# Optimization experiments

Measured on AMD Instinct MI355X. Metric: run time of the kernel, lower is better.

The kernel has to match this reference:

```python
import jax, jax.numpy as jnp
import numpy as np

N = 200000
E = 600000
H = 128
NUM_EDGE_TYPES = 16
LN_EPS = 1e-5


def setup_inputs() -> dict:
    key = jax.random.key(0)
    ks = jax.random.split(key, 10)
    x = jax.random.normal(ks[0], (N, H), dtype=jnp.float32)
    edge_index = jax.random.randint(ks[1], (2, E), 0, N, dtype=jnp.int32)
    edge_types = jax.random.randint(ks[2], (E,), 0, NUM_EDGE_TYPES, dtype=jnp.int32)
    s = 1.0 / np.sqrt(H)
    edge_emb = jax.random.normal(ks[3], (NUM_EDGE_TYPES, H), dtype=jnp.float32)
    W_self = jax.random.uniform(ks[4], (H, H), dtype=jnp.float32, minval=-s, maxval=s)
    b_self = jax.random.uniform(ks[5], (H,), dtype=jnp.float32, minval=-s, maxval=s)
    W_msg = jax.random.uniform(ks[6], (H, H), dtype=jnp.float32, minval=-s, maxval=s)
    b_msg = jax.random.uniform(ks[7], (H,), dtype=jnp.float32, minval=-s, maxval=s)
    gamma = jnp.ones((H,), dtype=jnp.float32)
    beta = jnp.zeros((H,), dtype=jnp.float32)
    return {
        "x": x, "edge_index": edge_index, "edge_types": edge_types,
        "edge_emb": edge_emb, "W_self": W_self, "b_self": b_self,
        "W_msg": W_msg, "b_msg": b_msg, "gamma": gamma, "beta": beta,
    }


def reference(x, edge_index, edge_types, edge_emb, W_self, b_self, W_msg, b_msg, gamma, beta):
    src = edge_index[0]
    dst = edge_index[1]
    # gather source node features + typed edge embedding: [E, H]
    typed_messages = x[src] + edge_emb[edge_types]
    # scatter-add into destination nodes: [N, H]
    aggregated = jnp.zeros_like(x).at[dst].add(typed_messages)
    # linear epilogue (torch Linear: y = x @ W.T + b)
    out = (x @ W_self.T + b_self) + (aggregated @ W_msg.T + b_msg)
    out = jax.nn.relu(out)
    # LayerNorm over last dim
    mu = jnp.mean(out, axis=-1, keepdims=True)
    var = jnp.mean(jnp.square(out - mu), axis=-1, keepdims=True)
    out = (out - mu) * jax.lax.rsqrt(var + LN_EPS) * gamma + beta
    # dropout is identity in eval mode
    return out
```

## Files before the change

kernel.cpp:

```cpp
#include <hip/hip_runtime.h>
#include <stdint.h>

#define H 128
#define TM 16
#define MAXDEG 24

typedef __attribute__((ext_vector_type(8))) short short8;
typedef __attribute__((ext_vector_type(4))) float f32x4;
typedef __attribute__((ext_vector_type(4))) int i32x4;

__device__ __forceinline__ unsigned short f2bf(float f) {
    union { float f; unsigned u; } v; v.f = f;
    unsigned u = v.u;
    u += 0x7fffu + ((u >> 16) & 1u);
    return (unsigned short)(u >> 16);
}

__device__ __forceinline__ float bf2f(unsigned short u) {
    union { unsigned u; float f; } v; v.u = ((unsigned)u) << 16; return v.f;
}

__device__ __forceinline__ short8 cvt8(f32x4 a, f32x4 b) {
    short8 r;
    r[0] = (short)f2bf(a.x); r[1] = (short)f2bf(a.y);
    r[2] = (short)f2bf(a.z); r[3] = (short)f2bf(a.w);
    r[4] = (short)f2bf(b.x); r[5] = (short)f2bf(b.y);
    r[6] = (short)f2bf(b.z); r[7] = (short)f2bf(b.w);
    return r;
}

__global__ __launch_bounds__(256) void prep_kernel(
    const float* __restrict__ x, const float* __restrict__ emb,
    unsigned short* __restrict__ xb, unsigned short* __restrict__ embb,
    const int* __restrict__ ei, const int* __restrict__ et,
    int* __restrict__ cnt, int* __restrict__ bucket,
    int total8x, int total8e, int E)
{
    int i = blockIdx.x * 256 + threadIdx.x;
    if (i < total8x) {
        f32x4 a = ((const f32x4*)x)[2 * i];
        f32x4 b = ((const f32x4*)x)[2 * i + 1];
        ((short8*)xb)[i] = cvt8(a, b);
    } else if (i < total8x + total8e) {
        int j = i - total8x;
        f32x4 a = ((const f32x4*)emb)[2 * j];
        f32x4 b = ((const f32x4*)emb)[2 * j + 1];
        ((short8*)embb)[j] = cvt8(a, b);
    }
    if (i < E) {
        int src = ei[i];
        int dst = ei[E + i];
        int t   = et[i];
        int pos = atomicAdd(&cnt[dst], 1);
        if (pos < MAXDEG) bucket[(size_t)dst * MAXDEG + pos] = src | (t << 18);
    }
}

template<bool EMB_LDS>
__global__ __launch_bounds__(256) void fused_gemm_kernel(
    const unsigned short* __restrict__ xb, const unsigned short* __restrict__ embb,
    const int* __restrict__ cnt, const int* __restrict__ bucket,
    const int* __restrict__ ei, const int* __restrict__ et,
    const float* __restrict__ Wself, const float* __restrict__ bself,
    const float* __restrict__ Wmsg, const float* __restrict__ bmsg,
    const float* __restrict__ gamma, const float* __restrict__ beta,
    float* __restrict__ out, int nTiles, int E, int T)
{
    __shared__ __align__(16) short a_stage[TM * 264];
    __shared__ __align__(16) float o_stage[TM * 132];
    __shared__ __align__(16) short emb_s[16 * 136];

    const int tid  = threadIdx.x;
    const int wave = tid >> 6;
    const int lane = tid & 63;
    const int col  = lane & 15;
    const int quad = lane >> 4;
    const int node = tid >> 4;
    const int l    = tid & 15;

    if (EMB_LDS && tid < T * 16) {
        int t = tid >> 4;
        *(short8*)&emb_s[t * 136 + l * 8] = *(const short8*)(embb + t * H + l * 8);
    }

    short8 bfrag[2][8];
    float bias[2];
#pragma unroll
    for (int s = 0; s < 2; ++s) {
        const int h = (wave * 2 + s) * 16 + col;
        bias[s] = bself[h] + bmsg[h];
#pragma unroll
        for (int kst = 0; kst < 8; ++kst) {
            const float* W = (kst < 4) ? Wself : Wmsg;
            const int k0 = (kst & 3) * 32 + quad * 8;
            const float* p = W + (size_t)h * H + k0;
            f32x4 w0 = *(const f32x4*)(p);
            f32x4 w1 = *(const f32x4*)(p + 4);
            bfrag[s][kst] = cvt8(w0, w1);
        }
    }

    const int f0 = l * 8;
    f32x4 g0  = *(const f32x4*)(gamma + f0);
    f32x4 g1  = *(const f32x4*)(gamma + f0 + 4);
    f32x4 be0 = *(const f32x4*)(beta + f0);
    f32x4 be1 = *(const f32x4*)(beta + f0 + 4);

    __syncthreads();

    for (int tile = blockIdx.x; tile < nTiles; tile += gridDim.x) {
        const size_t row = (size_t)tile * TM + node;

        short8 xv_st = *(const short8*)(xb + row * H + l * 8);

        int c = cnt[row];
        float acc[8] = {0.f, 0.f, 0.f, 0.f, 0.f, 0.f, 0.f, 0.f};
        if (c <= MAXDEG) {
            const int* b = bucket + row * MAXDEG;
            for (int i0 = 0; i0 < c; i0 += 4) {
                i32x4 p = *(const i32x4*)(b + i0);
                int rem = c - i0;
                bool h1 = rem > 1, h2 = rem > 2, h3 = rem > 3;
                short8 xv0, xv1, xv2, xv3, ev0, ev1, ev2, ev3;
                {
                    int s = p.x & 0x3FFFF, t = p.x >> 18;
                    xv0 = *(const short8*)(xb + (size_t)s * H + l * 8);
                    ev0 = EMB_LDS ? *(const short8*)&emb_s[t * 136 + l * 8]
                                  : *(const short8*)(embb + (size_t)t * H + l * 8);
                }
                if (h1) {
                    int s = p.y & 0x3FFFF, t = p.y >> 18;
                    xv1 = *(const short8*)(xb + (size_t)s * H + l * 8);
                    ev1 = EMB_LDS ? *(const short8*)&emb_s[t * 136 + l * 8]
                                  : *(const short8*)(embb + (size_t)t * H + l * 8);
                }
                if (h2) {
                    int s = p.z & 0x3FFFF, t = p.z >> 18;
                    xv2 = *(const short8*)(xb + (size_t)s * H + l * 8);
                    ev2 = EMB_LDS ? *(const short8*)&emb_s[t * 136 + l * 8]
                                  : *(const short8*)(embb + (size_t)t * H + l * 8);
                }
                if (h3) {
                    int s = p.w & 0x3FFFF, t = p.w >> 18;
                    xv3 = *(const short8*)(xb + (size_t)s * H + l * 8);
                    ev3 = EMB_LDS ? *(const short8*)&emb_s[t * 136 + l * 8]
                                  : *(const short8*)(embb + (size_t)t * H + l * 8);
                }
#pragma unroll
                for (int j = 0; j < 8; ++j) acc[j] += bf2f((unsigned short)xv0[j]) + bf2f((unsigned short)ev0[j]);
                if (h1) {
#pragma unroll
                    for (int j = 0; j < 8; ++j) acc[j] += bf2f((unsigned short)xv1[j]) + bf2f((unsigned short)ev1[j]);
                }
                if (h2) {
#pragma unroll
                    for (int j = 0; j < 8; ++j) acc[j] += bf2f((unsigned short)xv2[j]) + bf2f((unsigned short)ev2[j]);
                }
                if (h3) {
#pragma unroll
                    for (int j = 0; j < 8; ++j) acc[j] += bf2f((unsigned short)xv3[j]) + bf2f((unsigned short)ev3[j]);
                }
            }
        } else {
            for (int e = 0; e < E; ++e) {
                if (ei[E + e] == (int)row) {
                    int s = ei[e], t = et[e];
                    short8 xv = *(const short8*)(xb + (size_t)s * H + l * 8);
                    short8 ev = EMB_LDS ? *(const short8*)&emb_s[t * 136 + l * 8]
                                        : *(const short8*)(embb + (size_t)t * H + l * 8);
#pragma unroll
                    for (int j = 0; j < 8; ++j) acc[j] += bf2f((unsigned short)xv[j]) + bf2f((unsigned short)ev[j]);
                }
            }
        }

        *(short8*)&a_stage[node * 264 + l * 8] = xv_st;
        short8 ar;
#pragma unroll
        for (int j = 0; j < 8; ++j) ar[j] = (short)f2bf(acc[j]);
        *(short8*)&a_stage[node * 264 + 128 + l * 8] = ar;
        __syncthreads();

        short8 afr[8];
#pragma unroll
        for (int kst = 0; kst < 8; ++kst)
            afr[kst] = *(const short8*)(&a_stage[col * 264 + kst * 32 + quad * 8]);

        f32x4 acc0 = {0.f, 0.f, 0.f, 0.f};
        f32x4 acc1 = {0.f, 0.f, 0.f, 0.f};
#pragma unroll
        for (int kst = 0; kst < 8; ++kst) {
            acc0 = __builtin_amdgcn_mfma_f32_16x16x32_bf16(afr[kst], bfrag[0][kst], acc0, 0, 0, 0);
            acc1 = __builtin_amdgcn_mfma_f32_16x16x32_bf16(afr[kst], bfrag[1][kst], acc1, 0, 0, 0);
        }

#pragma unroll
        for (int s = 0; s < 2; ++s) {
            const int h = (wave * 2 + s) * 16 + col;
            f32x4 a = s ? acc1 : acc0;
#pragma unroll
            for (int r = 0; r < 4; ++r) {
                const int m = quad * 4 + r;
                float v = a[r] + bias[s];
                o_stage[m * 132 + h] = v > 0.f ? v : 0.f;
            }
        }
        __syncthreads();

        float v[8];
        float s1 = 0.f, s2 = 0.f;
#pragma unroll
        for (int j = 0; j < 8; ++j) {
            v[j] = o_stage[node * 132 + f0 + j];
            s1 += v[j];
            s2 += v[j] * v[j];
        }
#pragma unroll
        for (int m = 1; m < 16; m <<= 1) {
            s1 += __shfl_xor(s1, m, 64);
            s2 += __shfl_xor(s2, m, 64);
        }
        const float mu = s1 * (1.f / 128.f);
        const float var = s2 * (1.f / 128.f) - mu * mu;
        const float rstd = rsqrtf(var + 1e-5f);

        f32x4 o0, o1;
        o0.x = (v[0] - mu) * rstd * g0.x + be0.x;
        o0.y = (v[1] - mu) * rstd * g0.y + be0.y;
        o0.z = (v[2] - mu) * rstd * g0.z + be0.z;
        o0.w = (v[3] - mu) * rstd * g0.w + be0.w;
        o1.x = (v[4] - mu) * rstd * g1.x + be1.x;
        o1.y = (v[5] - mu) * rstd * g1.y + be1.y;
        o1.z = (v[6] - mu) * rstd * g1.z + be1.z;
        o1.w = (v[7] - mu) * rstd * g1.w + be1.w;

        float* dst = out + row * H + f0;
        __builtin_nontemporal_store(o0, (f32x4*)dst);
        __builtin_nontemporal_store(o1, (f32x4*)(dst + 4));
    }
}

__global__ __launch_bounds__(256) void scatter_kernel(
    const float* __restrict__ x, const int* __restrict__ ei,
    const int* __restrict__ et, const float* __restrict__ emb,
    float* __restrict__ agg, int E)
{
    int g = blockIdx.x * 256 + threadIdx.x;
    int e = g >> 5;
    int l = g & 31;
    if (e >= E) return;
    int src = ei[e];
    int dst = ei[E + e];
    int t   = et[e];
    f32x4 xv = *(const f32x4*)(x   + (size_t)src * H + l * 4);
    f32x4 ev = *(const f32x4*)(emb + (size_t)t   * H + l * 4);
    float* b = agg + (size_t)dst * H + l * 4;
    atomicAdd(b + 0, xv.x + ev.x);
    atomicAdd(b + 1, xv.y + ev.y);
    atomicAdd(b + 2, xv.z + ev.z);
    atomicAdd(b + 3, xv.w + ev.w);
}

__global__ __launch_bounds__(256) void gemm_ln_f32_kernel(
    const float* __restrict__ x,
    const float* __restrict__ Wself, const float* __restrict__ bself,
    const float* __restrict__ Wmsg, const float* __restrict__ bmsg,
    const float* __restrict__ gamma, const float* __restrict__ beta,
    float* __restrict__ out, int nTiles)
{
    __shared__ __align__(16) short a_stage[TM * 264];
    __shared__ __align__(16) float o_stage[TM * 132];

    const int tid  = threadIdx.x;
    const int wave = tid >> 6;
    const int lane = tid & 63;
    const int col  = lane & 15;
    const int quad = lane >> 4;

    short8 bfrag[2][8];
    float bias[2];
#pragma unroll
    for (int s = 0; s < 2; ++s) {
        const int h = (wave * 2 + s) * 16 + col;
        bias[s] = bself[h] + bmsg[h];
#pragma unroll
        for (int kst = 0; kst < 8; ++kst) {
            const float* W = (kst < 4) ? Wself : Wmsg;
            const int k0 = (kst & 3) * 32 + quad * 8;
            const float* p = W + (size_t)h * H + k0;
            f32x4 w0 = *(const f32x4*)(p);
            f32x4 w1 = *(const f32x4*)(p + 4);
            bfrag[s][kst] = cvt8(w0, w1);
        }
    }

    const int lnode = tid >> 4;
    const int f0 = (tid & 15) * 8;
    f32x4 g0  = *(const f32x4*)(gamma + f0);
    f32x4 g1  = *(const f32x4*)(gamma + f0 + 4);
    f32x4 be0 = *(const f32x4*)(beta + f0);
    f32x4 be1 = *(const f32x4*)(beta + f0 + 4);

    for (int tile = blockIdx.x; tile < nTiles; tile += gridDim.x) {
        const size_t rowBase = (size_t)tile * TM;
        {
            const int node = tid >> 4;
            const int seg  = tid & 15;
            const int k0   = seg * 16;
            const float* src = (seg < 8)
                ? (x   + (rowBase + node) * H + k0)
                : (out + (rowBase + node) * H + (k0 - 128));
            f32x4 v0 = ((const f32x4*)src)[0];
            f32x4 v1 = ((const f32x4*)src)[1];
            f32x4 v2 = ((const f32x4*)src)[2];
            f32x4 v3 = ((const f32x4*)src)[3];
            *(short8*)(&a_stage[node * 264 + k0])     = cvt8(v0, v1);
            *(short8*)(&a_stage[node * 264 + k0 + 8]) = cvt8(v2, v3);
        }
        __syncthreads();

        short8 afr[8];
#pragma unroll
        for (int kst = 0; kst < 8; ++kst)
            afr[kst] = *(const short8*)(&a_stage[col * 264 + kst * 32 + quad * 8]);

        f32x4 acc0 = {0.f, 0.f, 0.f, 0.f};
        f32x4 acc1 = {0.f, 0.f, 0.f, 0.f};
#pragma unroll
        for (int kst = 0; kst < 8; ++kst) {
            acc0 = __builtin_amdgcn_mfma_f32_16x16x32_bf16(afr[kst], bfrag[0][kst], acc0, 0, 0, 0);
            acc1 = __builtin_amdgcn_mfma_f32_16x16x32_bf16(afr[kst], bfrag[1][kst], acc1, 0, 0, 0);
        }

#pragma unroll
        for (int s = 0; s < 2; ++s) {
            const int h = (wave * 2 + s) * 16 + col;
            f32x4 a = s ? acc1 : acc0;
#pragma unroll
            for (int r = 0; r < 4; ++r) {
                const int m = quad * 4 + r;
                float v = a[r] + bias[s];
                o_stage[m * 132 + h] = v > 0.f ? v : 0.f;
            }
        }
        __syncthreads();

        float v[8];
        float s1 = 0.f, s2 = 0.f;
#pragma unroll
        for (int j = 0; j < 8; ++j) {
            v[j] = o_stage[lnode * 132 + f0 + j];
            s1 += v[j];
            s2 += v[j] * v[j];
        }
#pragma unroll
        for (int m = 1; m < 16; m <<= 1) {
            s1 += __shfl_xor(s1, m, 64);
            s2 += __shfl_xor(s2, m, 64);
        }
        const float mu = s1 * (1.f / 128.f);
        const float var = s2 * (1.f / 128.f) - mu * mu;
        const float rstd = rsqrtf(var + 1e-5f);

        f32x4 o0, o1;
        o0.x = (v[0] - mu) * rstd * g0.x + be0.x;
        o0.y = (v[1] - mu) * rstd * g0.y + be0.y;
        o0.z = (v[2] - mu) * rstd * g0.z + be0.z;
        o0.w = (v[3] - mu) * rstd * g0.w + be0.w;
        o1.x = (v[4] - mu) * rstd * g1.x + be1.x;
        o1.y = (v[5] - mu) * rstd * g1.y + be1.y;
        o1.z = (v[6] - mu) * rstd * g1.z + be1.z;
        o1.w = (v[7] - mu) * rstd * g1.w + be1.w;

        float* dst = out + (rowBase + lnode) * H + f0;
        *(f32x4*)(dst)     = o0;
        *(f32x4*)(dst + 4) = o1;
    }
}

extern "C" void kernel_launch(void* const* d_in, const int* in_sizes, int n_in,
                              void* d_out, int out_size, void* d_ws, size_t ws_size,
                              hipStream_t stream) {
    const float* x     = (const float*)d_in[0];
    const int*   ei    = (const int*)d_in[1];
    const int*   et    = (const int*)d_in[2];
    const float* emb   = (const float*)d_in[3];
    const float* Wself = (const float*)d_in[4];
    const float* bself = (const float*)d_in[5];
    const float* Wmsg  = (const float*)d_in[6];
    const float* bmsg  = (const float*)d_in[7];
    const float* gamma = (const float*)d_in[8];
    const float* beta  = (const float*)d_in[9];
    float* out = (float*)d_out;

    const int E = in_sizes[2];
    const int N = in_sizes[0] / H;
    const int T = in_sizes[3] / H;
    const int nTiles = N / TM;

    auto rnd = [](size_t b) { return (b + 255) & ~(size_t)255; };
    const size_t sz_xb   = rnd((size_t)N * H * 2);
    const size_t sz_embb = rnd((size_t)T * H * 2);
    const size_t sz_cnt  = rnd((size_t)N * 4);
    const size_t sz_bkt  = rnd((size_t)N * MAXDEG * 4);
    const size_t needA = sz_xb + sz_embb + sz_cnt + sz_bkt;

    const bool tierA = (ws_size >= needA) && (N <= (1 << 18)) && (T <= 4096)
                       && (N % TM == 0);

    if (tierA) {
        uint8_t* p = (uint8_t*)d_ws;
        unsigned short* xb   = (unsigned short*)p;  p += sz_xb;
        unsigned short* embb = (unsigned short*)p;  p += sz_embb;
        int* cnt    = (int*)p;                      p += sz_cnt;
        int* bucket = (int*)p;

        hipMemsetAsync(cnt, 0, (size_t)N * sizeof(int), stream);

        const int t8x = N * H / 8, t8e = T * H / 8;
        int prepWork = (t8x + t8e) > E ? (t8x + t8e) : E;
        prep_kernel<<<(prepWork + 255) / 256, 256, 0, stream>>>(
            x, emb, xb, embb, ei, et, cnt, bucket, t8x, t8e, E);

        int grid = 3125;
        if (grid > nTiles) grid = nTiles;
        if (T <= 16) {
            fused_gemm_kernel<true><<<grid, 256, 0, stream>>>(
                xb, embb, cnt, bucket, ei, et,
                Wself, bself, Wmsg, bmsg, gamma, beta, out, nTiles, E, T);
        } else {
            fused_gemm_kernel<false><<<grid, 256, 0, stream>>>(
                xb, embb, cnt, bucket, ei, et,
                Wself, bself, Wmsg, bmsg, gamma, beta, out, nTiles, E, T);
        }
    } else {
        hipMemsetAsync(out, 0, (size_t)N * H * sizeof(float), stream);
        const long long sthreads = (long long)E * 32;
        scatter_kernel<<<(int)((sthreads + 255) / 256), 256, 0, stream>>>(
            x, ei, et, emb, out, E);
        int grid = 2500;
        if (grid > nTiles) grid = nTiles;
        gemm_ln_f32_kernel<<<grid, 256, 0, stream>>>(
            x, Wself, bself, Wmsg, bmsg, gamma, beta, out, nTiles);
    }
}
```

Before: 335.8 us.

## Merge prep and fused GEMM into one cooperative kernel with grid sync

Replaces the separate prep and fused GEMM launches with a single cooperative persistent kernel. It converts x to bf16 and builds the per-destination buckets with grid-stride loops, then runs a grid-wide sync before the gather/GEMM/LayerNorm phase. It also lowers MAXDEG to 16, drops the bf16 embedding buffer by converting the embeddings straight into LDS, and preloads the first bucket quad ahead of the degree loop. The aim is to remove a launch boundary and its tail. The costs are an occupancy-limited grid, a grid-barrier, host occupancy/property queries on every call, and more nodes falling into the slow overflow path because of the smaller MAXDEG.

```diff
diff --git a/kernel.cpp b/kernel.cpp
--- a/kernel.cpp
+++ b/kernel.cpp
@@ -1,13 +1,22 @@
 #include <hip/hip_runtime.h>
+#include <hip/hip_cooperative_groups.h>
 #include <stdint.h>
+
+namespace cg = cooperative_groups;
 
 #define H 128
 #define TM 16
-#define MAXDEG 24
+#define MAXDEG 16
 
 typedef __attribute__((ext_vector_type(8))) short short8;
 typedef __attribute__((ext_vector_type(4))) float f32x4;
 typedef __attribute__((ext_vector_type(4))) int i32x4;
+
+struct SmemT {
+    short a_stage[TM * 264];
+    float o_stage[TM * 132];
+    short emb_s[16 * 136];
+};
 
 __device__ __forceinline__ unsigned short f2bf(float f) {
     union { float f; unsigned u; } v; v.f = f;
@@ -29,36 +38,32 @@
     return r;
 }
 
-__global__ __launch_bounds__(256) void prep_kernel(
-    const float* __restrict__ x, const float* __restrict__ emb,
-    unsigned short* __restrict__ xb, unsigned short* __restrict__ embb,
-    const int* __restrict__ ei, const int* __restrict__ et,
-    int* __restrict__ cnt, int* __restrict__ bucket,
-    int total8x, int total8e, int E)
-{
-    int i = blockIdx.x * 256 + threadIdx.x;
-    if (i < total8x) {
+__device__ __forceinline__ void dev_convert_x(
+    const float* __restrict__ x, unsigned short* __restrict__ xb,
+    int t8x, int gtid, int gsize)
+{
+    for (int i = gtid; i < t8x; i += gsize) {
         f32x4 a = ((const f32x4*)x)[2 * i];
         f32x4 b = ((const f32x4*)x)[2 * i + 1];
         ((short8*)xb)[i] = cvt8(a, b);
-    } else if (i < total8x + total8e) {
-        int j = i - total8x;
-        f32x4 a = ((const f32x4*)emb)[2 * j];
-        f32x4 b = ((const f32x4*)emb)[2 * j + 1];
-        ((short8*)embb)[j] = cvt8(a, b);
-    }
-    if (i < E) {
-        int src = ei[i];
-        int dst = ei[E + i];
-        int t   = et[i];
+    }
+}
+
+__device__ __forceinline__ void dev_build(
+    const int* __restrict__ ei, const int* __restrict__ et,
+    int* __restrict__ cnt, int* __restrict__ bucket, int E, int gtid, int gsize)
+{
+    for (int e = gtid; e < E; e += gsize) {
+        int src = ei[e];
+        int dst = ei[E + e];
+        int t   = et[e];
         int pos = atomicAdd(&cnt[dst], 1);
         if (pos < MAXDEG) bucket[(size_t)dst * MAXDEG + pos] = src | (t << 18);
     }
 }
 
-template<bool EMB_LDS>
-__global__ __launch_bounds__(256) void fused_gemm_kernel(
-    const unsigned short* __restrict__ xb, const unsigned short* __restrict__ embb,
+__device__ void dev_phase2(SmemT& sm,
+    const unsigned short* __restrict__ xb, const float* __restrict__ emb,
     const int* __restrict__ cnt, const int* __restrict__ bucket,
     const int* __restrict__ ei, const int* __restrict__ et,
     const float* __restrict__ Wself, const float* __restrict__ bself,
@@ -66,10 +71,6 @@
     const float* __restrict__ gamma, const float* __restrict__ beta,
     float* __restrict__ out, int nTiles, int E, int T)
 {
-    __shared__ __align__(16) short a_stage[TM * 264];
-    __shared__ __align__(16) float o_stage[TM * 132];
-    __shared__ __align__(16) short emb_s[16 * 136];
-
     const int tid  = threadIdx.x;
     const int wave = tid >> 6;
     const int lane = tid & 63;
@@ -77,10 +78,13 @@
     const int quad = lane >> 4;
     const int node = tid >> 4;
     const int l    = tid & 15;
-
-    if (EMB_LDS && tid < T * 16) {
-        int t = tid >> 4;
-        *(short8*)&emb_s[t * 136 + l * 8] = *(const short8*)(embb + t * H + l * 8);
+    const int f0   = l * 8;
+
+    if (tid < T * 16) {
+        const float* p = emb + (tid >> 4) * H + (tid & 15) * 8;
+        f32x4 a = *(const f32x4*)p;
+        f32x4 b = *(const f32x4*)(p + 4);
+        *(short8*)&sm.emb_s[(tid >> 4) * 136 + (tid & 15) * 8] = cvt8(a, b);
     }
 
     short8 bfrag[2][8];
@@ -100,7 +104,6 @@
         }
     }
 
-    const int f0 = l * 8;
     f32x4 g0  = *(const f32x4*)(gamma + f0);
     f32x4 g1  = *(const f32x4*)(gamma + f0 + 4);
     f32x4 be0 = *(const f32x4*)(beta + f0);
@@ -111,40 +114,75 @@
     for (int tile = blockIdx.x; tile < nTiles; tile += gridDim.x) {
         const size_t row = (size_t)tile * TM + node;
 
-        short8 xv_st = *(const short8*)(xb + row * H + l * 8);
-
+        short8 xv_st = *(const short8*)(xb + row * H + f0);
+        const int* brow = bucket + row * MAXDEG;
+        i32x4 p = *(const i32x4*)brow;
         int c = cnt[row];
+
         float acc[8] = {0.f, 0.f, 0.f, 0.f, 0.f, 0.f, 0.f, 0.f};
         if (c <= MAXDEG) {
-            const int* b = bucket + row * MAXDEG;
-            for (int i0 = 0; i0 < c; i0 += 4) {
-                i32x4 p = *(const i32x4*)(b + i0);
+            if (c > 0) {
+                bool h1 = c > 1, h2 = c > 2, h3 = c > 3;
+                short8 xv0, xv1, xv2, xv3, ev0, ev1, ev2, ev3;
+                {
+                    int s = p.x & 0x3FFFF, t = p.x >> 18;
+                    xv0 = *(const short8*)(xb + (size_t)s * H + f0);
+                    ev0 = *(const short8*)&sm.emb_s[t * 136 + f0];
+                }
+                if (h1) {
+                    int s = p.y & 0x3FFFF, t = p.y >> 18;
+                    xv1 = *(const short8*)(xb + (size_t)s * H + f0);
+                    ev1 = *(const short8*)&sm.emb_s[t * 136 + f0];
+                }
+                if (h2) {
+                    int s = p.z & 0x3FFFF, t = p.z >> 18;
+                    xv2 = *(const short8*)(xb + (size_t)s * H + f0);
+                    ev2 = *(const short8*)&sm.emb_s[t * 136 + f0];
+                }
+                if (h3) {
+                    int s = p.w & 0x3FFFF, t = p.w >> 18;
+                    xv3 = *(const short8*)(xb + (size_t)s * H + f0);
+                    ev3 = *(const short8*)&sm.emb_s[t * 136 + f0];
+                }
+#pragma unroll
+                for (int j = 0; j < 8; ++j) acc[j] += bf2f((unsigned short)xv0[j]) + bf2f((unsigned short)ev0[j]);
+                if (h1) {
+#pragma unroll
+                    for (int j = 0; j < 8; ++j) acc[j] += bf2f((unsigned short)xv1[j]) + bf2f((unsigned short)ev1[j]);
+                }
+                if (h2) {
+#pragma unroll
+                    for (int j = 0; j < 8; ++j) acc[j] += bf2f((unsigned short)xv2[j]) + bf2f((unsigned short)ev2[j]);
+                }
+                if (h3) {
+#pragma unroll
+                    for (int j = 0; j < 8; ++j) acc[j] += bf2f((unsigned short)xv3[j]) + bf2f((unsigned short)ev3[j]);
+                }
+            }
+            for (int i0 = 4; i0 < c; i0 += 4) {
+                i32x4 q = *(const i32x4*)(brow + i0);
                 int rem = c - i0;
                 bool h1 = rem > 1, h2 = rem > 2, h3 = rem > 3;
                 short8 xv0, xv1, xv2, xv3, ev0, ev1, ev2, ev3;
                 {
-                    int s = p.x & 0x3FFFF, t = p.x >> 18;
-                    xv0 = *(const short8*)(xb + (size_t)s * H + l * 8);
-                    ev0 = EMB_LDS ? *(const short8*)&emb_s[t * 136 + l * 8]
-                                  : *(const short8*)(embb + (size_t)t * H + l * 8);
+                    int s = q.x & 0x3FFFF, t = q.x >> 18;
+                    xv0 = *(const short8*)(xb + (size_t)s * H + f0);
+                    ev0 = *(const short8*)&sm.emb_s[t * 136 + f0];
                 }
                 if (h1) {
-                    int s = p.y & 0x3FFFF, t = p.y >> 18;
-                    xv1 = *(const short8*)(xb + (size_t)s * H + l * 8);
-                    ev1 = EMB_LDS ? *(const short8*)&emb_s[t * 136 + l * 8]
-                                  : *(const short8*)(embb + (size_t)t * H + l * 8);
+                    int s = q.y & 0x3FFFF, t = q.y >> 18;
+                    xv1 = *(const short8*)(xb + (size_t)s * H + f0);
+                    ev1 = *(const short8*)&sm.emb_s[t * 136 + f0];
                 }
                 if (h2) {
-                    int s = p.z & 0x3FFFF, t = p.z >> 18;
-                    xv2 = *(const short8*)(xb + (size_t)s * H + l * 8);
-                    ev2 = EMB_LDS ? *(const short8*)&emb_s[t * 136 + l * 8]
-                                  : *(const short8*)(embb + (size_t)t * H + l * 8);
+                    int s = q.z & 0x3FFFF, t = q.z >> 18;
+                    xv2 = *(const short8*)(xb + (size_t)s * H + f0);
+                    ev2 = *(const short8*)&sm.emb_s[t * 136 + f0];
                 }
                 if (h3) {
-                    int s = p.w & 0x3FFFF, t = p.w >> 18;
-                    xv3 = *(const short8*)(xb + (size_t)s * H + l * 8);
-                    ev3 = EMB_LDS ? *(const short8*)&emb_s[t * 136 + l * 8]
-                                  : *(const short8*)(embb + (size_t)t * H + l * 8);
+                    int s = q.w & 0x3FFFF, t = q.w >> 18;
+                    xv3 = *(const short8*)(xb + (size_t)s * H + f0);
+                    ev3 = *(const short8*)&sm.emb_s[t * 136 + f0];
                 }
 #pragma unroll
                 for (int j = 0; j < 8; ++j) acc[j] += bf2f((unsigned short)xv0[j]) + bf2f((unsigned short)ev0[j]);
@@ -165,26 +203,25 @@
             for (int e = 0; e < E; ++e) {
                 if (ei[E + e] == (int)row) {
                     int s = ei[e], t = et[e];
-                    short8 xv = *(const short8*)(xb + (size_t)s * H + l * 8);
-                    short8 ev = EMB_LDS ? *(const short8*)&emb_s[t * 136 + l * 8]
-                                        : *(const short8*)(embb + (size_t)t * H + l * 8);
+                    short8 xv = *(const short8*)(xb + (size_t)s * H + f0);
+                    short8 ev = *(const short8*)&sm.emb_s[t * 136 + f0];
 #pragma unroll
                     for (int j = 0; j < 8; ++j) acc[j] += bf2f((unsigned short)xv[j]) + bf2f((unsigned short)ev[j]);
                 }
             }
         }
 
-        *(short8*)&a_stage[node * 264 + l * 8] = xv_st;
+        *(short8*)&sm.a_stage[node * 264 + f0] = xv_st;
         short8 ar;
 #pragma unroll
         for (int j = 0; j < 8; ++j) ar[j] = (short)f2bf(acc[j]);
-        *(short8*)&a_stage[node * 264 + 128 + l * 8] = ar;
+        *(short8*)&sm.a_stage[node * 264 + 128 + f0] = ar;
         __syncthreads();
 
         short8 afr[8];
 #pragma unroll
         for (int kst = 0; kst < 8; ++kst)
-            afr[kst] = *(const short8*)(&a_stage[col * 264 + kst * 32 + quad * 8]);
+            afr[kst] = *(const short8*)(&sm.a_stage[col * 264 + kst * 32 + quad * 8]);
 
         f32x4 acc0 = {0.f, 0.f, 0.f, 0.f};
         f32x4 acc1 = {0.f, 0.f, 0.f, 0.f};
@@ -202,7 +239,7 @@
             for (int r = 0; r < 4; ++r) {
                 const int m = quad * 4 + r;
                 float v = a[r] + bias[s];
-                o_stage[m * 132 + h] = v > 0.f ? v : 0.f;
+                sm.o_stage[m * 132 + h] = v > 0.f ? v : 0.f;
             }
         }
         __syncthreads();
@@ -211,7 +248,7 @@
         float s1 = 0.f, s2 = 0.f;
 #pragma unroll
         for (int j = 0; j < 8; ++j) {
-            v[j] = o_stage[node * 132 + f0 + j];
+            v[j] = sm.o_stage[node * 132 + f0 + j];
             s1 += v[j];
             s2 += v[j] * v[j];
         }
@@ -238,6 +275,51 @@
         __builtin_nontemporal_store(o0, (f32x4*)dst);
         __builtin_nontemporal_store(o1, (f32x4*)(dst + 4));
     }
+}
+
+__global__ __launch_bounds__(256) void mono_kernel(
+    const float* __restrict__ x, const float* __restrict__ emb,
+    const int* __restrict__ ei, const int* __restrict__ et,
+    unsigned short* __restrict__ xb, int* __restrict__ cnt,
+    int* __restrict__ bucket,
+    const float* __restrict__ Wself, const float* __restrict__ bself,
+    const float* __restrict__ Wmsg, const float* __restrict__ bmsg,
+    const float* __restrict__ gamma, const float* __restrict__ beta,
+    float* __restrict__ out, int N, int E, int T, int nTiles)
+{
+    __shared__ SmemT sm;
+    const int gsize = gridDim.x * 256;
+    const int gtid  = blockIdx.x * 256 + threadIdx.x;
+    dev_convert_x(x, xb, N * (H / 8), gtid, gsize);
+    dev_build(ei, et, cnt, bucket, E, gtid, gsize);
+    cg::this_grid().sync();
+    dev_phase2(sm, xb, emb, cnt, bucket, ei, et,
+               Wself, bself, Wmsg, bmsg, gamma, beta, out, nTiles, E, T);
+}
+
+__global__ __launch_bounds__(256) void prep_kernel(
+    const float* __restrict__ x, const int* __restrict__ ei,
+    const int* __restrict__ et, unsigned short* __restrict__ xb,
+    int* __restrict__ cnt, int* __restrict__ bucket, int N, int E)
+{
+    const int gsize = gridDim.x * 256;
+    const int gtid  = blockIdx.x * 256 + threadIdx.x;
+    dev_convert_x(x, xb, N * (H / 8), gtid, gsize);
+    dev_build(ei, et, cnt, bucket, E, gtid, gsize);
+}
+
+__global__ __launch_bounds__(256) void fused_kernel(
+    const unsigned short* __restrict__ xb, const float* __restrict__ emb,
+    const int* __restrict__ cnt, const int* __restrict__ bucket,
+    const int* __restrict__ ei, const int* __restrict__ et,
+    const float* __restrict__ Wself, const float* __restrict__ bself,
+    const float* __restrict__ Wmsg, const float* __restrict__ bmsg,
+    const float* __restrict__ gamma, const float* __restrict__ beta,
+    float* __restrict__ out, int nTiles, int E, int T)
+{
+    __shared__ SmemT sm;
+    dev_phase2(sm, xb, emb, cnt, bucket, ei, et,
+               Wself, bself, Wmsg, bmsg, gamma, beta, out, nTiles, E, T);
 }
 
 __global__ __launch_bounds__(256) void scatter_kernel(
@@ -399,38 +481,58 @@
     const int nTiles = N / TM;
 
     auto rnd = [](size_t b) { return (b + 255) & ~(size_t)255; };
-    const size_t sz_xb   = rnd((size_t)N * H * 2);
-    const size_t sz_embb = rnd((size_t)T * H * 2);
-    const size_t sz_cnt  = rnd((size_t)N * 4);
-    const size_t sz_bkt  = rnd((size_t)N * MAXDEG * 4);
-    const size_t needA = sz_xb + sz_embb + sz_cnt + sz_bkt;
-
-    const bool tierA = (ws_size >= needA) && (N <= (1 << 18)) && (T <= 4096)
+    const size_t sz_xb  = rnd((size_t)N * H * 2);
+    const size_t sz_cnt = rnd((size_t)N * 4);
+    const size_t sz_bkt = rnd((size_t)N * MAXDEG * 4);
+    const size_t need = sz_xb + sz_cnt + sz_bkt;
+
+    const bool tierA = (ws_size >= need) && (N <= (1 << 18)) && (T <= 16)
                        && (N % TM == 0);
 
     if (tierA) {
         uint8_t* p = (uint8_t*)d_ws;
-        unsigned short* xb   = (unsigned short*)p;  p += sz_xb;
-        unsigned short* embb = (unsigned short*)p;  p += sz_embb;
-        int* cnt    = (int*)p;                      p += sz_cnt;
+        unsigned short* xb = (unsigned short*)p;  p += sz_xb;
+        int* cnt    = (int*)p;                    p += sz_cnt;
         int* bucket = (int*)p;
 
         hipMemsetAsync(cnt, 0, (size_t)N * sizeof(int), stream);
 
-        const int t8x = N * H / 8, t8e = T * H / 8;
-        int prepWork = (t8x + t8e) > E ? (t8x + t8e) : E;
-        prep_kernel<<<(prepWork + 255) / 256, 256, 0, stream>>>(
-            x, emb, xb, embb, ei, et, cnt, bucket, t8x, t8e, E);
-
-        int grid = 3125;
-        if (grid > nTiles) grid = nTiles;
-        if (T <= 16) {
-            fused_gemm_kernel<true><<<grid, 256, 0, stream>>>(
-                xb, embb, cnt, bucket, ei, et,
-                Wself, bself, Wmsg, bmsg, gamma, beta, out, nTiles, E, T);
-        } else {
-            fused_gemm_kernel<false><<<grid, 256, 0, stream>>>(
-                xb, embb, cnt, bucket, ei, et,
+        bool coop_done = false;
+        int maxB = 0;
+        hipError_t oe = hipOccupancyMaxActiveBlocksPerMultiprocessor(
+            &maxB, reinterpret_cast<const void*>(mono_kernel), 256, 0);
+        if (oe == hipSuccess && maxB > 0) {
+            hipDeviceProp_t props;
+            int dev = 0;
+            if (hipGetDevice(&dev) == hipSuccess &&
+                hipGetDeviceProperties(&props, dev) == hipSuccess) {
+                long long grid = (long long)maxB * props.multiProcessorCount;
+                if (grid > 65535) grid = 65535;
+                if (grid >= 64) {
+                    int Ni = N, Ei = E, Ti = T, nT = nTiles;
+                    void* args[] = {
+                        (void*)&x, (void*)&emb, (void*)&ei, (void*)&et,
+                        (void*)&xb, (void*)&cnt, (void*)&bucket,
+                        (void*)&Wself, (void*)&bself, (void*)&Wmsg, (void*)&bmsg,
+                        (void*)&gamma, (void*)&beta, (void*)&out,
+                        (void*)&Ni, (void*)&Ei, (void*)&Ti, (void*)&nT };
+                    hipError_t le = hipLaunchCooperativeKernel(
+                        reinterpret_cast<const void*>(mono_kernel),
+                        dim3((unsigned)grid), dim3(256), args, 0, stream);
+                    coop_done = (le == hipSuccess);
+                }
+            }
+        }
+
+        if (!coop_done) {
+            const int t8x = N * (H / 8);
+            int prepWork = t8x > E ? t8x : E;
+            prep_kernel<<<(prepWork + 255) / 256, 256, 0, stream>>>(
+                x, ei, et, xb, cnt, bucket, N, E);
+            int grid = 3125;
+            if (grid > nTiles) grid = nTiles;
+            fused_kernel<<<grid, 256, 0, stream>>>(
+                xb, emb, cnt, bucket, ei, et,
                 Wself, bself, Wmsg, bmsg, gamma, beta, out, nTiles, E, T);
         }
     } else {
```

Result: slower. 460.5 us (+37.2%).
